# Performance work log

Hardware: AMD Instinct MI355X
Metric: run time of the kernel (lower is better)

The kernel has to match this reference:

```python
import jax, jax.numpy as jnp
import numpy as np

B, L, H = 2, 2048, 1024
NH, HD = 16, 64  # n_heads, head_size


def setup_inputs() -> dict:
    key = jax.random.key(0)
    ks = jax.random.split(key, 12)
    scale = 1.0 / np.sqrt(H)
    inp = {
        "hidden_states": jax.random.normal(ks[0], (B, L, H), dtype=jnp.float32),
        "tau": jax.random.uniform(ks[1], (B, 1), dtype=jnp.float32) + 0.5,
        "delta": jax.random.normal(ks[2], (B, L), dtype=jnp.float32) * 0.1,
        "Wq": jax.random.normal(ks[3], (H, H), dtype=jnp.float32) * scale,
        "bq": jnp.zeros((H,), dtype=jnp.float32),
        "Wk": jax.random.normal(ks[4], (H, H), dtype=jnp.float32) * scale,
        "bk": jnp.zeros((H,), dtype=jnp.float32),
        "Wv": jax.random.normal(ks[5], (H, H), dtype=jnp.float32) * scale,
        "bv": jnp.zeros((H,), dtype=jnp.float32),
        "Wo": jax.random.normal(ks[6], (H, H), dtype=jnp.float32) * scale,
        "bo": jnp.zeros((H,), dtype=jnp.float32),
    }
    return inp


def _split_heads(x):
    # [B, L, H] -> [B, NH, L, HD]
    return x.reshape(B, L, NH, HD).transpose(0, 2, 1, 3)


def reference(hidden_states, tau, delta, Wq, bq, Wk, bk, Wv, bv, Wo, bo):
    q = _split_heads(hidden_states @ Wq.T + bq)
    k = _split_heads(hidden_states @ Wk.T + bk)
    v = _split_heads(hidden_states @ Wv.T + bv)
    tau_b = tau[:, :, None, None]          # [B,1,1,1]
    delta_b = delta[:, None, None, :]      # [B,1,1,L]
    scores = jnp.einsum('bhqd,bhkd->bhqk', q, k) * tau_b + delta_b
    scores = scores / np.sqrt(HD)
    attn = jax.nn.softmax(scores, axis=-1)  # dropout = identity (eval mode)
    ctx = jnp.einsum('bhqk,bhkd->bhqd', attn, v)
    ctx = ctx.transpose(0, 2, 1, 3).reshape(B, L, H)
    return ctx @ Wo.T + bo
```

## Files before the change

kernel.cpp:

```cpp
#include <hip/hip_runtime.h>

#define B_ 2
#define L_ 2048
#define H_ 1024
#define NH_ 16
#define HD_ 64

using short8 = __attribute__((__ext_vector_type__(8))) short;
using f32x4 = __attribute__((__ext_vector_type__(4))) float;
using f32x16 = __attribute__((__ext_vector_type__(16))) float;
typedef unsigned short u16;
typedef unsigned int u32;

__device__ __forceinline__ u16 f2bf(float f) {
  union { float f; unsigned u; } x{f};
  unsigned u = x.u;
  u = u + 0x7FFFu + ((u >> 16) & 1u);
  return (u16)(u >> 16);
}

__device__ __forceinline__ void gld16(const void* g, void* l) {
  __builtin_amdgcn_global_load_lds(
      (const __attribute__((address_space(1))) void*)g,
      (__attribute__((address_space(3))) void*)l, 16, 0, 0);
}

#define MFMA16(a, b, c) __builtin_amdgcn_mfma_f32_16x16x32_bf16((a), (b), (c), 0, 0, 0)
#define MFMA32(a, b, c) __builtin_amdgcn_mfma_f32_32x32x16_bf16((a), (b), (c), 0, 0, 0)

__global__ void cast_all(const float* __restrict__ hs, const float* __restrict__ Wq,
                         const float* __restrict__ Wk, const float* __restrict__ Wv,
                         const float* __restrict__ Wo, const float* __restrict__ delta,
                         u16* __restrict__ dst, float* __restrict__ dsc) {
  const int t = blockIdx.x * 256 + threadIdx.x;
  const int i = t * 4;
  const float* src;
  int off;
  if (i < 4194304) {
    src = hs; off = i;
  } else {
    const int j = i - 4194304;
    const int w = j >> 20;
    off = j & 1048575;
    src = (w == 0) ? Wq : (w == 1) ? Wk : (w == 2) ? Wv : Wo;
  }
  float4 v = *(const float4*)(src + off);
  *(ushort4*)(dst + i) = make_ushort4(f2bf(v.x), f2bf(v.y), f2bf(v.z), f2bf(v.w));
  if (t < 4096) dsc[t] = delta[t] * 0.18033688011112042f;
}

__global__ __launch_bounds__(512) void gemm_qkv256(
    const u16* __restrict__ A, const u16* __restrict__ W,
    const float* __restrict__ bq, const float* __restrict__ bk, const float* __restrict__ bv,
    const float* __restrict__ tau,
    u16* __restrict__ qg, u16* __restrict__ kg, u16* __restrict__ vTg) {
  __shared__ u16 As[2][256 * 64];
  __shared__ u16 Bs[2][256 * 64];
  const int tid = threadIdx.x;
  const int lane = tid & 63;
  const int wid = tid >> 6;
  const int wr = wid >> 2;
  const int wc = wid & 3;
  const int orig = blockIdx.y * 12 + blockIdx.x;
  const int wg = (orig & 7) * 24 + (orig >> 3);
  const int m0 = (wg & 15) * 256;
  const int n0 = (wg >> 4) * 256;

  const int srow = tid >> 3;
  const int sg = tid & 7;

#define STAGE256(slot, t_)                                                              \
  {                                                                                     \
    const int kt64 = (t_) * 64;                                                         \
    _Pragma("unroll") for (int li = 0; li < 4; li++) {                                  \
      const int row = li * 64 + srow;                                                   \
      const int gsrc = sg ^ (row & 7);                                                  \
      gld16(A + (size_t)(m0 + row) * 1024 + kt64 + gsrc * 8,                            \
            (char*)As[slot] + li * 8192 + wid * 1024 + lane * 16);                      \
      gld16(W + (size_t)(n0 + row) * 1024 + kt64 + gsrc * 8,                            \
            (char*)Bs[slot] + li * 8192 + wid * 1024 + lane * 16);                      \
    }                                                                                   \
  }

  f32x4 acc[8][4] = {};

  STAGE256(0, 0);
  STAGE256(1, 1);

  for (int t = 0; t < 16; t++) {
    if (t >= 1 && t + 1 < 16) STAGE256((t + 1) & 1, t + 1);
    if (t + 1 < 16) {
      asm volatile("s_waitcnt vmcnt(8)" ::: "memory");
    } else {
      asm volatile("s_waitcnt vmcnt(0)" ::: "memory");
    }
    asm volatile("s_barrier" ::: "memory");
    const u16* Ab = As[t & 1];
    const u16* Bb = Bs[t & 1];
    short8 bf[4];
#pragma unroll
    for (int q = 0; q < 4; q++) {
      const int mh = q & 1, ks = q >> 1;
      const int g0 = ks * 4 + (lane >> 4);
      if (mh == 0) {
#pragma unroll
        for (int ni = 0; ni < 4; ni++) {
          const int r = wc * 64 + ni * 16 + (lane & 15);
          bf[ni] = *(const short8*)((const char*)Bb + r * 128 + ((g0 ^ (r & 7)) << 4));
        }
      }
      short8 af[4];
#pragma unroll
      for (int mi = 0; mi < 4; mi++) {
        const int r = wr * 128 + (mh * 4 + mi) * 16 + (lane & 15);
        af[mi] = *(const short8*)((const char*)Ab + r * 128 + ((g0 ^ (r & 7)) << 4));
      }
      __builtin_amdgcn_s_setprio(1);
#pragma unroll
      for (int mi = 0; mi < 4; mi++)
#pragma unroll
        for (int ni = 0; ni < 4; ni++)
          acc[mh * 4 + mi][ni] = MFMA16(af[mi], bf[ni], acc[mh * 4 + mi][ni]);
      __builtin_amdgcn_s_setprio(0);
      asm volatile("s_barrier" ::: "memory");
    }
  }

  const int which = n0 >> 10;
  const int b_blk = m0 >> 11;
  const float scl = (which == 0) ? tau[b_blk] * 0.18033688011112042f : 1.0f;
  const float* bias = which == 0 ? bq : (which == 1 ? bk : bv);
#pragma unroll
  for (int ni = 0; ni < 4; ni++) {
    const int n = n0 + wc * 64 + ni * 16 + (lane & 15);
    const int nn = n & 1023;
    const int h = nn >> 6, d = nn & 63;
    const float bb = bias[nn];
#pragma unroll
    for (int mi = 0; mi < 8; mi++) {
      const int mb = m0 + wr * 128 + mi * 16 + ((lane >> 4) << 2);
      const int b = mb >> 11;
      const int lq = mb & 2047;
      if (which == 2) {
        ushort4 pk = make_ushort4(f2bf(acc[mi][ni][0] + bb), f2bf(acc[mi][ni][1] + bb),
                                  f2bf(acc[mi][ni][2] + bb), f2bf(acc[mi][ni][3] + bb));
        *(ushort4*)&vTg[((size_t)(b * NH_ + h) * HD_ + d) * L_ + lq] = pk;
      } else {
        u16* dst = which == 0 ? qg : kg;
#pragma unroll
        for (int r = 0; r < 4; r++)
          dst[((size_t)(b * NH_ + h) * L_ + lq + r) * HD_ + d] = f2bf((acc[mi][ni][r] + bb) * scl);
      }
    }
  }
}

__global__ __launch_bounds__(256) void attn(
    const u16* __restrict__ qg, const u16* __restrict__ kg, const u16* __restrict__ vTg,
    const float* __restrict__ dsc, u16* __restrict__ ctxg) {
  __shared__ u16 lds[2][8192];
  const int tid = threadIdx.x;
  const int lane = tid & 63;
  const int wv = tid >> 6;
  const int lane31 = lane & 31;
  const int hi = lane >> 5;
  const int orig = blockIdx.y * 16 + blockIdx.x;
  const int wgid = (orig & 7) * 64 + (orig >> 3);
  const int bh = wgid >> 4;
  const int qblk = wgid & 15;
  const int b = bh >> 4;
  const int h = bh & 15;
  const int q0 = qblk * 128 + wv * 32;
  const u16* qb = qg + (size_t)bh * L_ * HD_;
  const u16* kb = kg + (size_t)bh * L_ * HD_;
  const u16* vb = vTg + (size_t)bh * HD_ * L_;
  const float* db = dsc + (size_t)b * L_;

  short8 qf[4];
#pragma unroll
  for (int ks = 0; ks < 4; ks++)
    qf[ks] = *(const short8*)&qb[(size_t)(q0 + lane31) * 64 + ks * 16 + hi * 8];

  union { u32 u[4]; short8 s; } onesu;
  const u32 ow = (lane31 == 0) ? 0x3F803F80u : 0u;
  onesu.u[0] = ow; onesu.u[1] = ow; onesu.u[2] = ow; onesu.u[3] = ow;
  const short8 onesf = onesu.s;

  f32x16 acc[2] = {};
  f32x16 accl = {};
  float mrun = -__builtin_inff();

  const int i0 = 2 * wv, i1 = 2 * wv + 1;

#define STAGE(bufi, j0)                                                                   \
  {                                                                                       \
    u16* bp = lds[bufi];                                                                  \
    {                                                                                     \
      const int kt = i0 >> 2, ks = i0 & 3;                                                \
      gld16(kb + (size_t)((j0) + kt * 32 + lane31) * 64 + ks * 16 + hi * 8,               \
            bp + i0 * 512 + lane * 8);                                                    \
    }                                                                                     \
    {                                                                                     \
      const int kt = i1 >> 2, ks = i1 & 3;                                                \
      gld16(kb + (size_t)((j0) + kt * 32 + lane31) * 64 + ks * 16 + hi * 8,               \
            bp + i1 * 512 + lane * 8);                                                    \
    }                                                                                     \
    {                                                                                     \
      const int kt = i0 >> 2, dt = (i0 >> 1) & 1, ks2 = i0 & 1;                           \
      gld16(vb + (size_t)(dt * 32 + lane31) * L_ + (j0) + kt * 32 + ks2 * 16 + hi * 8,    \
            bp + (8 + i0) * 512 + lane * 8);                                              \
    }                                                                                     \
    {                                                                                     \
      const int kt = i1 >> 2, dt = (i1 >> 1) & 1, ks2 = i1 & 1;                           \
      gld16(vb + (size_t)(dt * 32 + lane31) * L_ + (j0) + kt * 32 + ks2 * 16 + hi * 8,    \
            bp + (8 + i1) * 512 + lane * 8);                                              \
    }                                                                                     \
  }

  STAGE(0, 0);
  __syncthreads();
  int cur = 0;
  for (int jt = 0; jt < L_ / 64; jt++) {
    const int j0 = jt * 64;
    if (jt + 1 < L_ / 64) STAGE(cur ^ 1, j0 + 64);
    const u16* bp = lds[cur];
#pragma unroll
    for (int kt = 0; kt < 2; kt++) {
      f32x16 s = {};
      __builtin_amdgcn_s_setprio(1);
#pragma unroll
      for (int ks = 0; ks < 4; ks++) {
        short8 kf = *(const short8*)&bp[(kt * 4 + ks) * 512 + lane * 8];
        s = MFMA32(kf, qf[ks], s);
      }
      __builtin_amdgcn_s_setprio(0);
      float sv[16];
#pragma unroll
      for (int g = 0; g < 4; g++) {
        float4 dl = *(const float4*)&db[j0 + kt * 32 + g * 8 + hi * 4];
        sv[g * 4 + 0] = s[g * 4 + 0] + dl.x;
        sv[g * 4 + 1] = s[g * 4 + 1] + dl.y;
        sv[g * 4 + 2] = s[g * 4 + 2] + dl.z;
        sv[g * 4 + 3] = s[g * 4 + 3] + dl.w;
      }
      float t0 = fmaxf(fmaxf(sv[0], sv[1]), fmaxf(sv[2], sv[3]));
      float t1 = fmaxf(fmaxf(sv[4], sv[5]), fmaxf(sv[6], sv[7]));
      float t2 = fmaxf(fmaxf(sv[8], sv[9]), fmaxf(sv[10], sv[11]));
      float t3 = fmaxf(fmaxf(sv[12], sv[13]), fmaxf(sv[14], sv[15]));
      float pmax = fmaxf(fmaxf(t0, t1), fmaxf(t2, t3));
      pmax = fmaxf(pmax, __shfl_xor(pmax, 32));
      if (!__all(pmax - mrun <= 11.5f)) {
        float mnew = fmaxf(mrun, pmax);
        float al = __builtin_amdgcn_exp2f(mrun - mnew);
        mrun = mnew;
        accl[0] *= al;
#pragma unroll
        for (int dt = 0; dt < 2; dt++)
#pragma unroll
          for (int r = 0; r < 16; r++) acc[dt][r] *= al;
      }
      float p[16];
#pragma unroll
      for (int r = 0; r < 16; r++) p[r] = __builtin_amdgcn_exp2f(sv[r] - mrun);
      u32 pk[8];
#pragma unroll
      for (int i = 0; i < 8; i++)
        asm("v_cvt_pk_bf16_f32 %0, %1, %2" : "=v"(pk[i]) : "v"(p[2 * i]), "v"(p[2 * i + 1]));
      asm volatile("v_permlane32_swap_b32 %0, %1" : "+v"(pk[0]), "+v"(pk[2]));
      asm volatile("v_permlane32_swap_b32 %0, %1" : "+v"(pk[1]), "+v"(pk[3]));
      asm volatile("v_permlane32_swap_b32 %0, %1" : "+v"(pk[4]), "+v"(pk[6]));
      asm volatile("v_permlane32_swap_b32 %0, %1" : "+v"(pk[5]), "+v"(pk[7]));
      union U8 { u32 u[4]; short8 s; } f0, f1;
      f0.u[0] = pk[0]; f0.u[1] = pk[1]; f0.u[2] = pk[2]; f0.u[3] = pk[3];
      f1.u[0] = pk[4]; f1.u[1] = pk[5]; f1.u[2] = pk[6]; f1.u[3] = pk[7];
      __builtin_amdgcn_s_setprio(1);
#pragma unroll
      for (int ks2 = 0; ks2 < 2; ks2++) {
        short8 pf = ks2 ? f1.s : f0.s;
#pragma unroll
        for (int dt = 0; dt < 2; dt++) {
          short8 vf = *(const short8*)&bp[(8 + kt * 4 + dt * 2 + ks2) * 512 + lane * 8];
          acc[dt] = MFMA32(vf, pf, acc[dt]);
        }
        accl = MFMA32(onesf, pf, accl);
      }
      __builtin_amdgcn_s_setprio(0);
    }
    __syncthreads();
    cur ^= 1;
  }

  __syncthreads();
  u16* tw = lds[0] + wv * 2048;
  const float l0 = accl[0];
  const float l1 = __shfl_xor(l0, 32);
  const float inv = 1.0f / (hi ? l1 : l0);
#pragma unroll
  for (int dt = 0; dt < 2; dt++)
#pragma unroll
    for (int g = 0; g < 4; g++) {
      ushort4 w4 = make_ushort4(f2bf(acc[dt][g * 4 + 0] * inv), f2bf(acc[dt][g * 4 + 1] * inv),
                                f2bf(acc[dt][g * 4 + 2] * inv), f2bf(acc[dt][g * 4 + 3] * inv));
      const int d0 = dt * 32 + g * 8 + hi * 4;
      const int byte = (lane31 * 128 + d0 * 2) ^ ((lane31 & 15) << 3);
      *(ushort4*)((char*)tw + byte) = w4;
    }
  asm volatile("s_waitcnt lgkmcnt(0)" ::: "memory");
  const size_t obase = ((size_t)b * L_ + q0) * 1024 + h * 64;
#pragma unroll
  for (int i = 0; i < 16; i++) {
    const int qr = 2 * i + hi;
    const int byte = (qr * 128 + lane31 * 4) ^ ((qr & 15) << 3);
    const u32 val = *(const u32*)((const char*)tw + byte);
    *(u32*)&ctxg[obase + (size_t)qr * 1024 + lane31 * 2] = val;
  }
}

__global__ __launch_bounds__(256) void gemm_out(
    const u16* __restrict__ A, const u16* __restrict__ W,
    const float* __restrict__ bo, float* __restrict__ out) {
  __shared__ u16 As[128 * 64];
  __shared__ u16 Bs[128 * 64];
  const int tid = threadIdx.x;
  const int lane = tid & 63;
  const int wave = tid >> 6;
  const int wrow = (wave >> 1) * 64;
  const int wcol = (wave & 1) * 64;
  const int m0 = blockIdx.y * 128;
  const int n0 = blockIdx.x * 128;
  const int rr = tid >> 3;
  const int c8 = (tid & 7) * 8;
  f32x4 acc[4][4] = {};
  for (int kt = 0; kt < 1024; kt += 64) {
#pragma unroll
    for (int i = 0; i < 4; i++) {
      gld16(A + (size_t)(m0 + i * 32 + rr) * 1024 + kt + c8, (char*)As + i * 4096 + wave * 1024);
      gld16(W + (size_t)(n0 + i * 32 + rr) * 1024 + kt + c8, (char*)Bs + i * 4096 + wave * 1024);
    }
    __syncthreads();
#pragma unroll
    for (int kc = 0; kc < 2; kc++) {
      const int ko = kc * 32 + (lane >> 4) * 8;
      short8 af[4], bf[4];
#pragma unroll
      for (int mi = 0; mi < 4; mi++)
        af[mi] = *(const short8*)&As[(wrow + mi * 16 + (lane & 15)) * 64 + ko];
#pragma unroll
      for (int ni = 0; ni < 4; ni++)
        bf[ni] = *(const short8*)&Bs[(wcol + ni * 16 + (lane & 15)) * 64 + ko];
#pragma unroll
      for (int mi = 0; mi < 4; mi++)
#pragma unroll
        for (int ni = 0; ni < 4; ni++)
          acc[mi][ni] = MFMA16(af[mi], bf[ni], acc[mi][ni]);
    }
    __syncthreads();
  }
#pragma unroll
  for (int ni = 0; ni < 4; ni++) {
    const int n = n0 + wcol + ni * 16 + (lane & 15);
    const float bb = bo[n];
#pragma unroll
    for (int mi = 0; mi < 4; mi++) {
      const int mb = m0 + wrow + mi * 16 + ((lane >> 4) << 2);
#pragma unroll
      for (int r = 0; r < 4; r++)
        out[(size_t)(mb + r) * 1024 + n] = acc[mi][ni][r] + bb;
    }
  }
}

extern "C" void kernel_launch(void* const* d_in, const int* in_sizes, int n_in,
                              void* d_out, int out_size, void* d_ws, size_t ws_size,
                              hipStream_t stream) {
  const float* hs = (const float*)d_in[0];
  const float* tau = (const float*)d_in[1];
  const float* delta = (const float*)d_in[2];
  const float* Wq = (const float*)d_in[3];
  const float* bq = (const float*)d_in[4];
  const float* Wk = (const float*)d_in[5];
  const float* bk = (const float*)d_in[6];
  const float* Wv = (const float*)d_in[7];
  const float* bv = (const float*)d_in[8];
  const float* Wo = (const float*)d_in[9];
  const float* bo = (const float*)d_in[10];
  float* out = (float*)d_out;

  u16* ws = (u16*)d_ws;
  u16* hsb  = ws;
  u16* wqkv = ws + 4194304;
  u16* wob  = ws + 7340032;
  u16* qg   = ws + 8388608;
  u16* kg   = ws + 12582912;
  u16* vTg  = ws + 16777216;
  u16* ctxg = ws + 20971520;
  float* dsc = (float*)(ws + 25165824);

  cast_all<<<8192, 256, 0, stream>>>(hs, Wq, Wk, Wv, Wo, delta, ws, dsc);

  gemm_qkv256<<<dim3(12, 16), 512, 0, stream>>>(hsb, wqkv, bq, bk, bv, tau, qg, kg, vTg);
  attn<<<dim3(16, 32), 256, 0, stream>>>(qg, kg, vTg, dsc, ctxg);
  gemm_out<<<dim3(8, 32), 256, 0, stream>>>(ctxg, wob, bo, out);
}
```

Measured before the change: 151.4 us.

## Restructure attention into single-wave blocks loading K/V directly to registers

The attention kernel changes from 256-thread blocks, which staged K/V tiles through double-buffered LDS with barriers, to 2048 one-wave blocks. Each wave now loads K and V fragments straight from global memory into registers, ping-ponging two register tile sets to prefetch. The row sum is now built from VALU adds and a cross-half shuffle instead of an extra MFMA against a ones vector. This removes LDS staging and block-wide barriers, but K/V reuse across the four waves of a block is lost, so global/L2 traffic rises about fourfold and more registers are needed per wave.

```diff
diff --git a/kernel.cpp b/kernel.cpp
--- a/kernel.cpp
+++ b/kernel.cpp
@@ -155,22 +155,20 @@
   }
 }
 
-__global__ __launch_bounds__(256) void attn(
+__global__ __launch_bounds__(64) void attn(
     const u16* __restrict__ qg, const u16* __restrict__ kg, const u16* __restrict__ vTg,
     const float* __restrict__ dsc, u16* __restrict__ ctxg) {
-  __shared__ u16 lds[2][8192];
-  const int tid = threadIdx.x;
-  const int lane = tid & 63;
-  const int wv = tid >> 6;
+  __shared__ u16 tw[2048];
+  const int lane = threadIdx.x;
   const int lane31 = lane & 31;
   const int hi = lane >> 5;
-  const int orig = blockIdx.y * 16 + blockIdx.x;
-  const int wgid = (orig & 7) * 64 + (orig >> 3);
-  const int bh = wgid >> 4;
-  const int qblk = wgid & 15;
+  const int orig = blockIdx.x;
+  const int wgid = (orig & 7) * 256 + (orig >> 3);
+  const int bh = wgid >> 6;
+  const int qblk = wgid & 63;
   const int b = bh >> 4;
   const int h = bh & 15;
-  const int q0 = qblk * 128 + wv * 32;
+  const int q0 = qblk * 32;
   const u16* qb = qg + (size_t)bh * L_ * HD_;
   const u16* kb = kg + (size_t)bh * L_ * HD_;
   const u16* vb = vTg + (size_t)bh * HD_ * L_;
@@ -181,120 +179,88 @@
   for (int ks = 0; ks < 4; ks++)
     qf[ks] = *(const short8*)&qb[(size_t)(q0 + lane31) * 64 + ks * 16 + hi * 8];
 
-  union { u32 u[4]; short8 s; } onesu;
-  const u32 ow = (lane31 == 0) ? 0x3F803F80u : 0u;
-  onesu.u[0] = ow; onesu.u[1] = ow; onesu.u[2] = ow; onesu.u[3] = ow;
-  const short8 onesf = onesu.s;
-
   f32x16 acc[2] = {};
-  f32x16 accl = {};
-  float mrun = -__builtin_inff();
-
-  const int i0 = 2 * wv, i1 = 2 * wv + 1;
-
-#define STAGE(bufi, j0)                                                                   \
-  {                                                                                       \
-    u16* bp = lds[bufi];                                                                  \
-    {                                                                                     \
-      const int kt = i0 >> 2, ks = i0 & 3;                                                \
-      gld16(kb + (size_t)((j0) + kt * 32 + lane31) * 64 + ks * 16 + hi * 8,               \
-            bp + i0 * 512 + lane * 8);                                                    \
-    }                                                                                     \
-    {                                                                                     \
-      const int kt = i1 >> 2, ks = i1 & 3;                                                \
-      gld16(kb + (size_t)((j0) + kt * 32 + lane31) * 64 + ks * 16 + hi * 8,               \
-            bp + i1 * 512 + lane * 8);                                                    \
-    }                                                                                     \
-    {                                                                                     \
-      const int kt = i0 >> 2, dt = (i0 >> 1) & 1, ks2 = i0 & 1;                           \
-      gld16(vb + (size_t)(dt * 32 + lane31) * L_ + (j0) + kt * 32 + ks2 * 16 + hi * 8,    \
-            bp + (8 + i0) * 512 + lane * 8);                                              \
-    }                                                                                     \
-    {                                                                                     \
-      const int kt = i1 >> 2, dt = (i1 >> 1) & 1, ks2 = i1 & 1;                           \
-      gld16(vb + (size_t)(dt * 32 + lane31) * L_ + (j0) + kt * 32 + ks2 * 16 + hi * 8,    \
-            bp + (8 + i1) * 512 + lane * 8);                                              \
-    }                                                                                     \
-  }
-
-  STAGE(0, 0);
-  __syncthreads();
-  int cur = 0;
-  for (int jt = 0; jt < L_ / 64; jt++) {
-    const int j0 = jt * 64;
-    if (jt + 1 < L_ / 64) STAGE(cur ^ 1, j0 + 64);
-    const u16* bp = lds[cur];
-#pragma unroll
-    for (int kt = 0; kt < 2; kt++) {
-      f32x16 s = {};
-      __builtin_amdgcn_s_setprio(1);
-#pragma unroll
-      for (int ks = 0; ks < 4; ks++) {
-        short8 kf = *(const short8*)&bp[(kt * 4 + ks) * 512 + lane * 8];
-        s = MFMA32(kf, qf[ks], s);
-      }
-      __builtin_amdgcn_s_setprio(0);
-      float sv[16];
-#pragma unroll
-      for (int g = 0; g < 4; g++) {
-        float4 dl = *(const float4*)&db[j0 + kt * 32 + g * 8 + hi * 4];
-        sv[g * 4 + 0] = s[g * 4 + 0] + dl.x;
-        sv[g * 4 + 1] = s[g * 4 + 1] + dl.y;
-        sv[g * 4 + 2] = s[g * 4 + 2] + dl.z;
-        sv[g * 4 + 3] = s[g * 4 + 3] + dl.w;
-      }
-      float t0 = fmaxf(fmaxf(sv[0], sv[1]), fmaxf(sv[2], sv[3]));
-      float t1 = fmaxf(fmaxf(sv[4], sv[5]), fmaxf(sv[6], sv[7]));
-      float t2 = fmaxf(fmaxf(sv[8], sv[9]), fmaxf(sv[10], sv[11]));
-      float t3 = fmaxf(fmaxf(sv[12], sv[13]), fmaxf(sv[14], sv[15]));
-      float pmax = fmaxf(fmaxf(t0, t1), fmaxf(t2, t3));
-      pmax = fmaxf(pmax, __shfl_xor(pmax, 32));
-      if (!__all(pmax - mrun <= 11.5f)) {
-        float mnew = fmaxf(mrun, pmax);
-        float al = __builtin_amdgcn_exp2f(mrun - mnew);
-        mrun = mnew;
-        accl[0] *= al;
-#pragma unroll
-        for (int dt = 0; dt < 2; dt++)
-#pragma unroll
-          for (int r = 0; r < 16; r++) acc[dt][r] *= al;
-      }
-      float p[16];
-#pragma unroll
-      for (int r = 0; r < 16; r++) p[r] = __builtin_amdgcn_exp2f(sv[r] - mrun);
-      u32 pk[8];
-#pragma unroll
-      for (int i = 0; i < 8; i++)
-        asm("v_cvt_pk_bf16_f32 %0, %1, %2" : "=v"(pk[i]) : "v"(p[2 * i]), "v"(p[2 * i + 1]));
-      asm volatile("v_permlane32_swap_b32 %0, %1" : "+v"(pk[0]), "+v"(pk[2]));
-      asm volatile("v_permlane32_swap_b32 %0, %1" : "+v"(pk[1]), "+v"(pk[3]));
-      asm volatile("v_permlane32_swap_b32 %0, %1" : "+v"(pk[4]), "+v"(pk[6]));
-      asm volatile("v_permlane32_swap_b32 %0, %1" : "+v"(pk[5]), "+v"(pk[7]));
-      union U8 { u32 u[4]; short8 s; } f0, f1;
-      f0.u[0] = pk[0]; f0.u[1] = pk[1]; f0.u[2] = pk[2]; f0.u[3] = pk[3];
-      f1.u[0] = pk[4]; f1.u[1] = pk[5]; f1.u[2] = pk[6]; f1.u[3] = pk[7];
-      __builtin_amdgcn_s_setprio(1);
-#pragma unroll
-      for (int ks2 = 0; ks2 < 2; ks2++) {
-        short8 pf = ks2 ? f1.s : f0.s;
-#pragma unroll
-        for (int dt = 0; dt < 2; dt++) {
-          short8 vf = *(const short8*)&bp[(8 + kt * 4 + dt * 2 + ks2) * 512 + lane * 8];
-          acc[dt] = MFMA32(vf, pf, acc[dt]);
-        }
-        accl = MFMA32(onesf, pf, accl);
-      }
-      __builtin_amdgcn_s_setprio(0);
-    }
-    __syncthreads();
-    cur ^= 1;
-  }
-
-  __syncthreads();
-  u16* tw = lds[0] + wv * 2048;
-  const float l0 = accl[0];
-  const float l1 = __shfl_xor(l0, 32);
-  const float inv = 1.0f / (hi ? l1 : l0);
+  float mrun = -__builtin_inff(), lrun = 0.f;
+
+#define LOADT(kf, vf, t_)                                                                \
+  {                                                                                      \
+    const int j = (t_) * 32;                                                             \
+    _Pragma("unroll") for (int ks = 0; ks < 4; ks++)                                     \
+        kf[ks] = *(const short8*)&kb[(size_t)(j + lane31) * 64 + ks * 16 + hi * 8];      \
+    _Pragma("unroll") for (int i = 0; i < 4; i++) {                                      \
+      const int dt = i >> 1, ks2 = i & 1;                                                \
+      vf[i] = *(const short8*)&vb[(size_t)(dt * 32 + lane31) * L_ + j + ks2 * 16 + hi * 8]; \
+    }                                                                                    \
+  }
+
+#define TILE(kf, vf, t_)                                                                 \
+  {                                                                                      \
+    const int j = (t_) * 32;                                                             \
+    f32x16 s = {};                                                                       \
+    __builtin_amdgcn_s_setprio(1);                                                       \
+    _Pragma("unroll") for (int ks = 0; ks < 4; ks++) s = MFMA32(kf[ks], qf[ks], s);      \
+    __builtin_amdgcn_s_setprio(0);                                                       \
+    float sv[16];                                                                        \
+    _Pragma("unroll") for (int g = 0; g < 4; g++) {                                      \
+      float4 dl = *(const float4*)&db[j + g * 8 + hi * 4];                               \
+      sv[g * 4 + 0] = s[g * 4 + 0] + dl.x;                                               \
+      sv[g * 4 + 1] = s[g * 4 + 1] + dl.y;                                               \
+      sv[g * 4 + 2] = s[g * 4 + 2] + dl.z;                                               \
+      sv[g * 4 + 3] = s[g * 4 + 3] + dl.w;                                               \
+    }                                                                                    \
+    float t0 = fmaxf(fmaxf(sv[0], sv[1]), fmaxf(sv[2], sv[3]));                          \
+    float t1 = fmaxf(fmaxf(sv[4], sv[5]), fmaxf(sv[6], sv[7]));                          \
+    float t2 = fmaxf(fmaxf(sv[8], sv[9]), fmaxf(sv[10], sv[11]));                        \
+    float t3 = fmaxf(fmaxf(sv[12], sv[13]), fmaxf(sv[14], sv[15]));                      \
+    float pmax = fmaxf(fmaxf(t0, t1), fmaxf(t2, t3));                                    \
+    pmax = fmaxf(pmax, __shfl_xor(pmax, 32));                                            \
+    if (!__all(pmax - mrun <= 11.5f)) {                                                  \
+      float mnew = fmaxf(mrun, pmax);                                                    \
+      float al = __builtin_amdgcn_exp2f(mrun - mnew);                                    \
+      mrun = mnew;                                                                       \
+      lrun *= al;                                                                        \
+      _Pragma("unroll") for (int dt = 0; dt < 2; dt++)                                   \
+          _Pragma("unroll") for (int r = 0; r < 16; r++) acc[dt][r] *= al;               \
+    }                                                                                    \
+    float p[16];                                                                         \
+    _Pragma("unroll") for (int r = 0; r < 16; r++)                                       \
+        p[r] = __builtin_amdgcn_exp2f(sv[r] - mrun);                                     \
+    float r0 = (p[0] + p[1]) + (p[2] + p[3]);                                            \
+    float r1 = (p[4] + p[5]) + (p[6] + p[7]);                                            \
+    float r2 = (p[8] + p[9]) + (p[10] + p[11]);                                          \
+    float r3 = (p[12] + p[13]) + (p[14] + p[15]);                                        \
+    float rs = (r0 + r1) + (r2 + r3);                                                    \
+    rs += __shfl_xor(rs, 32);                                                            \
+    lrun += rs;                                                                          \
+    u32 pk[8];                                                                           \
+    _Pragma("unroll") for (int i = 0; i < 8; i++)                                        \
+        asm("v_cvt_pk_bf16_f32 %0, %1, %2" : "=v"(pk[i]) : "v"(p[2 * i]), "v"(p[2 * i + 1])); \
+    asm volatile("v_permlane32_swap_b32 %0, %1" : "+v"(pk[0]), "+v"(pk[2]));             \
+    asm volatile("v_permlane32_swap_b32 %0, %1" : "+v"(pk[1]), "+v"(pk[3]));             \
+    asm volatile("v_permlane32_swap_b32 %0, %1" : "+v"(pk[4]), "+v"(pk[6]));             \
+    asm volatile("v_permlane32_swap_b32 %0, %1" : "+v"(pk[5]), "+v"(pk[7]));             \
+    union U8 { u32 u[4]; short8 s; } f0, f1;                                             \
+    f0.u[0] = pk[0]; f0.u[1] = pk[1]; f0.u[2] = pk[2]; f0.u[3] = pk[3];                  \
+    f1.u[0] = pk[4]; f1.u[1] = pk[5]; f1.u[2] = pk[6]; f1.u[3] = pk[7];                  \
+    __builtin_amdgcn_s_setprio(1);                                                       \
+    _Pragma("unroll") for (int ks2 = 0; ks2 < 2; ks2++) {                                \
+      short8 pf = ks2 ? f1.s : f0.s;                                                     \
+      _Pragma("unroll") for (int dt = 0; dt < 2; dt++)                                   \
+          acc[dt] = MFMA32(vf[dt * 2 + ks2], pf, acc[dt]);                               \
+    }                                                                                    \
+    __builtin_amdgcn_s_setprio(0);                                                       \
+  }
+
+  short8 kA[4], vA[4], kB[4], vB[4];
+  LOADT(kA, vA, 0);
+  for (int t = 0; t < 64; t += 2) {
+    LOADT(kB, vB, t + 1);
+    TILE(kA, vA, t);
+    if (t + 2 < 64) LOADT(kA, vA, t + 2);
+    TILE(kB, vB, t + 1);
+  }
+
+  const float inv = 1.0f / lrun;
 #pragma unroll
   for (int dt = 0; dt < 2; dt++)
 #pragma unroll
@@ -399,6 +365,6 @@
   cast_all<<<8192, 256, 0, stream>>>(hs, Wq, Wk, Wv, Wo, delta, ws, dsc);
 
   gemm_qkv256<<<dim3(12, 16), 512, 0, stream>>>(hsb, wqkv, bq, bk, bv, tau, qg, kg, vTg);
-  attn<<<dim3(16, 32), 256, 0, stream>>>(qg, kg, vTg, dsc, ctxg);
+  attn<<<2048, 64, 0, stream>>>(qg, kg, vTg, dsc, ctxg);
   gemm_out<<<dim3(8, 32), 256, 0, stream>>>(ctxg, wob, bo, out);
 }
```

Result: slower. 213.6 us (+41.1%).
